# Kernel optimization log

Hardware: AMD Instinct MI355X
Metric: run time of the kernel (lower is better)

## Reference

```python
import jax, jax.numpy as jnp
import numpy as np

DIM = 1024
INTER = 512
E = 16            # n_routed_experts
TOPK = 4          # n_activated_experts
N_GROUPS = 4
TOPK_GROUPS = 2
ROUTE_SCALE = 1.0
INIT_STD = 0.02
B, S = 2, 1024


def setup_inputs() -> dict:
    key = jax.random.key(0)
    ks = jax.random.split(key, 8)
    return {
        "x": jax.random.normal(ks[0], (B, S, DIM), jnp.float32),
        "gate_w": jax.random.normal(ks[1], (E, DIM), jnp.float32) * INIT_STD,
        "gate_bias": jnp.zeros((E,), jnp.float32),
        "w1": jax.random.normal(ks[2], (E, INTER, DIM), jnp.float32) * INIT_STD,
        "w2": jax.random.normal(ks[3], (E, DIM, INTER), jnp.float32) * INIT_STD,
        "w3": jax.random.normal(ks[4], (E, INTER, DIM), jnp.float32) * INIT_STD,
        "ws1": jax.random.normal(ks[5], (INTER, DIM), jnp.float32) * INIT_STD,
        "ws2": jax.random.normal(ks[6], (DIM, INTER), jnp.float32) * INIT_STD,
        "ws3": jax.random.normal(ks[7], (INTER, DIM), jnp.float32) * INIT_STD,
    }


def reference(x, gate_w, gate_bias, w1, w2, w3, ws1, ws2, ws3):
    Bx, Sx, D = x.shape
    T = Bx * Sx
    xf = x.reshape(T, D)

    # ---- Gate: sigmoid scores + expert bias, group-limited top-k ----
    scores = jax.nn.sigmoid(xf @ gate_w.T)          # [T, E]
    original_scores = scores
    s = scores + gate_bias                          # bias only affects selection
    sg = s.reshape(T, N_GROUPS, E // N_GROUPS)
    group_scores = sg.max(axis=-1)                  # [T, G]
    _, gidx = jax.lax.top_k(group_scores, TOPK_GROUPS)
    keep = jnp.zeros((T, N_GROUPS), bool).at[jnp.arange(T)[:, None], gidx].set(True)
    s_masked = jnp.where(keep[:, :, None], sg, -jnp.inf).reshape(T, E)
    _, idx = jax.lax.top_k(s_masked, TOPK)          # [T, topk]
    weights = jnp.take_along_axis(original_scores, idx, axis=1) * ROUTE_SCALE

    # combine weights as sparse [T, E] matrix (scatter of top-k weights)
    comb = jnp.zeros((T, E), x.dtype).at[jnp.arange(T)[:, None], idx].add(weights)

    # ---- Routed experts: SwiGLU per expert, weighted combine ----
    h1 = jnp.einsum('td,eid->tei', xf, w1)          # [T, E, inter]
    h3 = jnp.einsum('td,eid->tei', xf, w3)
    h = jax.nn.silu(h1) * h3
    y = jnp.einsum('tei,edi,te->td', h, w2, comb)   # weighted combine

    # ---- Shared expert (SwiGLU MLP) ----
    z = (jax.nn.silu(xf @ ws1.T) * (xf @ ws3.T)) @ ws2.T

    return (y + z).reshape(Bx, Sx, D)
```

## Files before the change

kernel.cpp:

```cpp
#include <hip/hip_runtime.h>

#define T_TOK  2048
#define DIMD   1024
#define INTERI 512
#define NEXP   16
#define NSEG   17

typedef __bf16 bf16x8 __attribute__((ext_vector_type(8)));
typedef float  f32x4  __attribute__((ext_vector_type(4)));

#define SW(row, c) ((((c) + ((row) >> 1)) & 3) * 8)

__device__ __forceinline__ unsigned short f2b(float f) {
    union { float f; unsigned int u; } c; c.f = f;
    unsigned int u = c.u;
    unsigned int r = (u + 0x7FFFu + ((u >> 16) & 1u)) >> 16;
    return (unsigned short)r;
}

__device__ __forceinline__ void lds_barrier() {
    asm volatile("s_waitcnt lgkmcnt(0)" ::: "memory");
    __builtin_amdgcn_s_barrier();
}

__global__ __launch_bounds__(256) void cvt_all_kernel(
    const float* __restrict__ x,  const float* __restrict__ w1,
    const float* __restrict__ w3, const float* __restrict__ w2,
    const float* __restrict__ ws1, const float* __restrict__ ws3,
    const float* __restrict__ ws2,
    unsigned short* __restrict__ xb,  unsigned short* __restrict__ w1b,
    unsigned short* __restrict__ w3b, unsigned short* __restrict__ w2b,
    unsigned short* __restrict__ ws1b, unsigned short* __restrict__ ws3b,
    unsigned short* __restrict__ ws2b)
{
    int g = blockIdx.x * 256 + threadIdx.x;
    const float* s; unsigned short* d; int i;
    if      (g < 524288)  { s = x;   d = xb;   i = g; }
    else if (g < 2621440) { s = w1;  d = w1b;  i = g - 524288; }
    else if (g < 4718592) { s = w3;  d = w3b;  i = g - 2621440; }
    else if (g < 6815744) { s = w2;  d = w2b;  i = g - 4718592; }
    else if (g < 6946816) { s = ws1; d = ws1b; i = g - 6815744; }
    else if (g < 7077888) { s = ws3; d = ws3b; i = g - 6946816; }
    else                  { s = ws2; d = ws2b; i = g - 7077888; }
    float4 v = ((const float4*)s)[i];
    ushort4 o;
    o.x = f2b(v.x); o.y = f2b(v.y); o.z = f2b(v.z); o.w = f2b(v.w);
    ((ushort4*)d)[i] = o;
}

__global__ __launch_bounds__(256) void gate_score_kernel(
    const float* __restrict__ x, const float* __restrict__ gw,
    const float* __restrict__ gb,
    unsigned* __restrict__ sel, float4* __restrict__ selw)
{
    int tok  = blockIdx.x * 4 + (threadIdx.x >> 6);
    int lane = threadIdx.x & 63;
    const float* xp = x + (size_t)tok * DIMD;
    float xv[16];
#pragma unroll
    for (int j = 0; j < 16; ++j) xv[j] = xp[j * 64 + lane];

    float sc[16];
#pragma unroll
    for (int e = 0; e < 16; ++e) {
        const float* gwe = gw + e * DIMD;
        float p0 = 0.f, p1 = 0.f;
#pragma unroll
        for (int j = 0; j < 16; j += 2) {
            p0 += xv[j]     * gwe[j * 64 + lane];
            p1 += xv[j + 1] * gwe[(j + 1) * 64 + lane];
        }
        float p = p0 + p1;
#pragma unroll
        for (int o = 32; o; o >>= 1) p += __shfl_xor(p, o, 64);
        sc[e] = p;
    }
    if (lane != 0) return;

    float orig[16], s[16];
#pragma unroll
    for (int e = 0; e < 16; ++e) {
        orig[e] = 1.f / (1.f + expf(-sc[e]));
        s[e] = orig[e] + gb[e];
    }
    float gmax[4];
#pragma unroll
    for (int g = 0; g < 4; ++g) {
        float m = s[4 * g];
        for (int j = 1; j < 4; ++j) m = fmaxf(m, s[4 * g + j]);
        gmax[g] = m;
    }
    int g0 = 0;
    for (int g = 1; g < 4; ++g) if (gmax[g] > gmax[g0]) g0 = g;
    int g1 = -1;
    for (int g = 0; g < 4; ++g) { if (g == g0) continue; if (g1 < 0 || gmax[g] > gmax[g1]) g1 = g; }
    unsigned keep = (0xFu << (4 * g0)) | (0xFu << (4 * g1));
    unsigned used = 0;
    unsigned pk = 0;
    float w4[4];
    for (int j = 0; j < 4; ++j) {
        int best = -1;
        for (int e = 0; e < 16; ++e) {
            if (!((keep >> e) & 1u) || ((used >> e) & 1u)) continue;
            if (best < 0 || s[e] > s[best]) best = e;
        }
        used |= 1u << best;
        pk |= ((unsigned)best) << (4 * j);
        w4[j] = orig[best];
    }
    sel[tok] = pk;
    selw[tok] = make_float4(w4[0], w4[1], w4[2], w4[3]);
}

__global__ __launch_bounds__(256) void build_lists_kernel(
    const unsigned* __restrict__ sel, const float4* __restrict__ selw,
    int* __restrict__ counts, int* __restrict__ lst, float* __restrict__ lstw)
{
    const int e    = blockIdx.x;
    const int tid  = threadIdx.x;
    const int wave = tid >> 6;
    const int lane = tid & 63;

    __shared__ int wsum[4];
    __shared__ int basev;
    if (tid == 0) basev = 0;
    __syncthreads();

    for (int c = 0; c < T_TOK / 256; ++c) {
        int t = c * 256 + tid;
        unsigned s = sel[t];
        int match = -1;
#pragma unroll
        for (int j = 0; j < 4; ++j)
            if (((s >> (4 * j)) & 15u) == (unsigned)e) match = j;
        unsigned long long m = __ballot(match >= 0);
        int wpre = __popcll(m & ((1ull << lane) - 1ull));
        if (lane == 0) wsum[wave] = __popcll(m);
        __syncthreads();
        int pre = basev;
        for (int wv = 0; wv < wave; ++wv) pre += wsum[wv];
        if (match >= 0) {
            int pos = pre + wpre;
            lst [e * T_TOK + pos] = t | (match << 16);
            const float* wp = (const float*)&selw[t];
            lstw[e * T_TOK + pos] = wp[match];
        }
        __syncthreads();
        if (tid == 0) basev += wsum[0] + wsum[1] + wsum[2] + wsum[3];
        __syncthreads();
    }
    if (tid == 0) counts[e] = basev;
}

__global__ __launch_bounds__(256, 2) void gemm1_kernel(
    const unsigned short* __restrict__ xb,
    const unsigned short* __restrict__ w1b,
    const unsigned short* __restrict__ w3b,
    const unsigned short* __restrict__ ws1b,
    const unsigned short* __restrict__ ws3b,
    const int* __restrict__ counts,
    const int* __restrict__ lst,
    unsigned short* __restrict__ H)
{
    int b = blockIdx.x;
    int seg, mt, nt;
    if (b < 1024) {
        int xcd = b & 7, slot = b >> 3;
        seg = xcd + 8 * (slot >> 6);
        int tile = slot & 63;
        mt = tile >> 2; nt = tile & 3;
    } else {
        seg = NEXP;
        int tile = b - 1024;
        mt = tile >> 2; nt = tile & 3;
    }
    const int n_e = (seg == NEXP) ? T_TOK : counts[seg];
    const int m0  = mt * 128;
    if (m0 >= n_e) return;
    const int n0  = nt * 128;

    const unsigned short* w1p = (seg == NEXP) ? ws1b : w1b + (size_t)seg * INTERI * DIMD;
    const unsigned short* w3p = (seg == NEXP) ? ws3b : w3b + (size_t)seg * INTERI * DIMD;
    const int* lste = lst + seg * T_TOK;

    __shared__ __align__(16) unsigned short lA [2][128][32];
    __shared__ __align__(16) unsigned short lB1[2][128][32];
    __shared__ __align__(16) unsigned short lB3[2][128][32];

    const int tid  = threadIdx.x;
    const int wave = tid >> 6;
    const int lane = tid & 63;
    const int quad = lane >> 4;
    const int lrow = lane & 15;
    const int r4   = tid >> 2;
    const int ct   = tid & 3;

    int ra0 = m0 + r4;       if (ra0 > n_e - 1) ra0 = n_e - 1;
    int ra1 = m0 + r4 + 64;  if (ra1 > n_e - 1) ra1 = n_e - 1;
    int tok0 = (seg == NEXP) ? ra0 : (lste[ra0] & 0xFFFF);
    int tok1 = (seg == NEXP) ? ra1 : (lste[ra1] & 0xFFFF);
    const unsigned short* gA0  = xb  + (size_t)tok0 * DIMD + ct * 8;
    const unsigned short* gA1  = xb  + (size_t)tok1 * DIMD + ct * 8;
    const unsigned short* gB1a = w1p + (size_t)(n0 + r4)      * DIMD + ct * 8;
    const unsigned short* gB1b = w1p + (size_t)(n0 + r4 + 64) * DIMD + ct * 8;
    const unsigned short* gB3a = w3p + (size_t)(n0 + r4)      * DIMD + ct * 8;
    const unsigned short* gB3b = w3p + (size_t)(n0 + r4 + 64) * DIMD + ct * 8;

    bf16x8 pa[2][2], pb1[2][2], pb3[2][2];

#define G1LOAD(k0) do { _Pragma("unroll") for (int kk = 0; kk < 2; ++kk) { \
    pa [0][kk] = *(const bf16x8*)(gA0  + (k0) + kk * 32); \
    pa [1][kk] = *(const bf16x8*)(gA1  + (k0) + kk * 32); \
    pb1[0][kk] = *(const bf16x8*)(gB1a + (k0) + kk * 32); \
    pb1[1][kk] = *(const bf16x8*)(gB1b + (k0) + kk * 32); \
    pb3[0][kk] = *(const bf16x8*)(gB3a + (k0) + kk * 32); \
    pb3[1][kk] = *(const bf16x8*)(gB3b + (k0) + kk * 32); } } while (0)

#define G1STORE() do { _Pragma("unroll") for (int kk = 0; kk < 2; ++kk) { \
    *(bf16x8*)&lA [kk][r4]     [SW(r4, ct)]      = pa [0][kk]; \
    *(bf16x8*)&lA [kk][64 + r4][SW(64 + r4, ct)] = pa [1][kk]; \
    *(bf16x8*)&lB1[kk][r4]     [SW(r4, ct)]      = pb1[0][kk]; \
    *(bf16x8*)&lB1[kk][64 + r4][SW(64 + r4, ct)] = pb1[1][kk]; \
    *(bf16x8*)&lB3[kk][r4]     [SW(r4, ct)]      = pb3[0][kk]; \
    *(bf16x8*)&lB3[kk][64 + r4][SW(64 + r4, ct)] = pb3[1][kk]; } } while (0)

    f32x4 acc1[4][4], acc3[4][4];
    const f32x4 zero = {0.f, 0.f, 0.f, 0.f};
#pragma unroll
    for (int i = 0; i < 4; ++i)
#pragma unroll
        for (int j = 0; j < 4; ++j) { acc1[i][j] = zero; acc3[i][j] = zero; }

    const int wm = (wave & 1) * 64;
    const int wn = (wave >> 1) * 64;

    G1LOAD(0);
    const int NK = DIMD / 64;
    for (int it = 0; it < NK; ++it) {
        G1STORE();
        lds_barrier();
        if (it + 1 < NK) G1LOAD((it + 1) * 64);
#pragma unroll
        for (int kk = 0; kk < 2; ++kk) {
            bf16x8 a[4], b1[4], b3[4];
#pragma unroll
            for (int t = 0; t < 4; ++t) {
                int rr = wm + t * 16 + lrow;
                a[t] = *(const bf16x8*)&lA[kk][rr][SW(rr, quad)];
            }
#pragma unroll
            for (int t = 0; t < 4; ++t) {
                int rc = wn + t * 16 + lrow;
                b1[t] = *(const bf16x8*)&lB1[kk][rc][SW(rc, quad)];
                b3[t] = *(const bf16x8*)&lB3[kk][rc][SW(rc, quad)];
            }
#pragma unroll
            for (int i = 0; i < 4; ++i)
#pragma unroll
                for (int j = 0; j < 4; ++j) {
                    acc1[i][j] = __builtin_amdgcn_mfma_f32_16x16x32_bf16(a[i], b1[j], acc1[i][j], 0, 0, 0);
                    acc3[i][j] = __builtin_amdgcn_mfma_f32_16x16x32_bf16(a[i], b3[j], acc3[i][j], 0, 0, 0);
                }
        }
        lds_barrier();
    }
#undef G1LOAD
#undef G1STORE

    unsigned short* Hseg = H + (size_t)seg * T_TOK * INTERI;
#pragma unroll
    for (int i = 0; i < 4; ++i) {
        int rbase = m0 + wm + i * 16 + quad * 4;
#pragma unroll
        for (int r = 0; r < 4; ++r) {
            int row = rbase + r;
            if (row >= n_e) continue;
            unsigned short* hrow = Hseg + (size_t)row * INTERI + n0 + wn + lrow;
#pragma unroll
            for (int j = 0; j < 4; ++j) {
                float v1 = acc1[i][j][r];
                float v3 = acc3[i][j][r];
                float hv = (v1 / (1.f + __expf(-v1))) * v3;
                hrow[j * 16] = f2b(hv);
            }
        }
    }
}

__global__ __launch_bounds__(256, 2) void gemm2_kernel(
    const unsigned short* __restrict__ H,
    const unsigned short* __restrict__ w2b,
    const unsigned short* __restrict__ ws2b,
    const int* __restrict__ counts,
    const int* __restrict__ lst,
    const float* __restrict__ lstw,
    float* __restrict__ P)
{
    int b = blockIdx.x;
    int seg, mt, nt;
    if (b < 2048) {
        int xcd = b & 7, slot = b >> 3;
        seg = xcd + 8 * (slot >> 7);
        int tile = slot & 127;
        mt = tile >> 3; nt = tile & 7;
    } else {
        seg = NEXP;
        int tile = b - 2048;
        mt = tile >> 3; nt = tile & 7;
    }
    const int n_e = (seg == NEXP) ? T_TOK : counts[seg];
    const int m0  = mt * 128;
    if (m0 >= n_e) return;
    const int n0  = nt * 128;

    const unsigned short* w2p  = (seg == NEXP) ? ws2b : w2b + (size_t)seg * DIMD * INTERI;
    const unsigned short* Hseg = H + (size_t)seg * T_TOK * INTERI;

    __shared__ __align__(16) unsigned short lA[2][128][32];
    __shared__ __align__(16) unsigned short lB[2][128][32];

    const int tid  = threadIdx.x;
    const int wave = tid >> 6;
    const int lane = tid & 63;
    const int quad = lane >> 4;
    const int lrow = lane & 15;
    const int r4   = tid >> 2;
    const int ct   = tid & 3;

    int ra0 = m0 + r4;       if (ra0 > n_e - 1) ra0 = n_e - 1;
    int ra1 = m0 + r4 + 64;  if (ra1 > n_e - 1) ra1 = n_e - 1;
    const unsigned short* gA0 = Hseg + (size_t)ra0 * INTERI + ct * 8;
    const unsigned short* gA1 = Hseg + (size_t)ra1 * INTERI + ct * 8;
    const unsigned short* gB0 = w2p + (size_t)(n0 + r4)      * INTERI + ct * 8;
    const unsigned short* gB1 = w2p + (size_t)(n0 + r4 + 64) * INTERI + ct * 8;

    bf16x8 pa[2][2], pb[2][2];

#define G2LOAD(k0) do { _Pragma("unroll") for (int kk = 0; kk < 2; ++kk) { \
    pa[0][kk] = *(const bf16x8*)(gA0 + (k0) + kk * 32); \
    pa[1][kk] = *(const bf16x8*)(gA1 + (k0) + kk * 32); \
    pb[0][kk] = *(const bf16x8*)(gB0 + (k0) + kk * 32); \
    pb[1][kk] = *(const bf16x8*)(gB1 + (k0) + kk * 32); } } while (0)

#define G2STORE() do { _Pragma("unroll") for (int kk = 0; kk < 2; ++kk) { \
    *(bf16x8*)&lA[kk][r4]     [SW(r4, ct)]      = pa[0][kk]; \
    *(bf16x8*)&lA[kk][64 + r4][SW(64 + r4, ct)] = pa[1][kk]; \
    *(bf16x8*)&lB[kk][r4]     [SW(r4, ct)]      = pb[0][kk]; \
    *(bf16x8*)&lB[kk][64 + r4][SW(64 + r4, ct)] = pb[1][kk]; } } while (0)

    f32x4 acc[4][4];
    const f32x4 zero = {0.f, 0.f, 0.f, 0.f};
#pragma unroll
    for (int i = 0; i < 4; ++i)
#pragma unroll
        for (int j = 0; j < 4; ++j) acc[i][j] = zero;

    const int wm = (wave & 1) * 64;
    const int wn = (wave >> 1) * 64;

    G2LOAD(0);
    const int NK = INTERI / 64;
    for (int it = 0; it < NK; ++it) {
        G2STORE();
        lds_barrier();
        if (it + 1 < NK) G2LOAD((it + 1) * 64);
#pragma unroll
        for (int kk = 0; kk < 2; ++kk) {
            bf16x8 a[4], bv[4];
#pragma unroll
            for (int t = 0; t < 4; ++t) {
                int rr = wm + t * 16 + lrow;
                a[t] = *(const bf16x8*)&lA[kk][rr][SW(rr, quad)];
            }
#pragma unroll
            for (int t = 0; t < 4; ++t) {
                int rc = wn + t * 16 + lrow;
                bv[t] = *(const bf16x8*)&lB[kk][rc][SW(rc, quad)];
            }
#pragma unroll
            for (int i = 0; i < 4; ++i)
#pragma unroll
                for (int j = 0; j < 4; ++j)
                    acc[i][j] = __builtin_amdgcn_mfma_f32_16x16x32_bf16(a[i], bv[j], acc[i][j], 0, 0, 0);
        }
        lds_barrier();
    }
#undef G2LOAD
#undef G2STORE

#pragma unroll
    for (int i = 0; i < 4; ++i) {
        int rbase = m0 + wm + i * 16 + quad * 4;
#pragma unroll
        for (int r = 0; r < 4; ++r) {
            int row = rbase + r;
            if (row >= n_e) continue;
            int tok, slot; float wt;
            if (seg == NEXP) { tok = row; slot = 4; wt = 1.f; }
            else {
                int ent = lst[seg * T_TOK + row];
                tok = ent & 0xFFFF; slot = ent >> 16;
                wt = lstw[seg * T_TOK + row];
            }
            float* prow = P + ((size_t)slot * T_TOK + tok) * DIMD + n0 + wn + lrow;
#pragma unroll
            for (int j = 0; j < 4; ++j)
                prow[j * 16] = wt * acc[i][j][r];
        }
    }
}

__global__ __launch_bounds__(256) void combine_kernel(
    const float4* __restrict__ P, float4* __restrict__ y)
{
    const int i = blockIdx.x * 256 + threadIdx.x;
    const size_t plane = (size_t)T_TOK * DIMD / 4;
    float4 a = P[i];
    float4 b = P[plane + i];
    float4 c = P[2 * plane + i];
    float4 d = P[3 * plane + i];
    float4 e = P[4 * plane + i];
    float4 o;
    o.x = a.x + b.x + c.x + d.x + e.x;
    o.y = a.y + b.y + c.y + d.y + e.y;
    o.z = a.z + b.z + c.z + d.z + e.z;
    o.w = a.w + b.w + c.w + d.w + e.w;
    y[i] = o;
}

extern "C" void kernel_launch(void* const* d_in, const int* in_sizes, int n_in,
                              void* d_out, int out_size, void* d_ws, size_t ws_size,
                              hipStream_t stream)
{
    const float* x   = (const float*)d_in[0];
    const float* gw  = (const float*)d_in[1];
    const float* gb  = (const float*)d_in[2];
    const float* w1  = (const float*)d_in[3];
    const float* w2  = (const float*)d_in[4];
    const float* w3  = (const float*)d_in[5];
    const float* ws1 = (const float*)d_in[6];
    const float* ws2 = (const float*)d_in[7];
    const float* ws3 = (const float*)d_in[8];

    char* base = (char*)d_ws;
    size_t off = 0;
    auto alloc = [&](size_t bytes) {
        char* q = base + off; off += (bytes + 255) & ~(size_t)255; return q;
    };
    unsigned short* xb   = (unsigned short*)alloc((size_t)T_TOK * DIMD * 2);
    unsigned short* w1b  = (unsigned short*)alloc((size_t)NEXP * INTERI * DIMD * 2);
    unsigned short* w3b  = (unsigned short*)alloc((size_t)NEXP * INTERI * DIMD * 2);
    unsigned short* w2b  = (unsigned short*)alloc((size_t)NEXP * DIMD * INTERI * 2);
    unsigned short* ws1b = (unsigned short*)alloc((size_t)INTERI * DIMD * 2);
    unsigned short* ws3b = (unsigned short*)alloc((size_t)INTERI * DIMD * 2);
    unsigned short* ws2b = (unsigned short*)alloc((size_t)DIMD * INTERI * 2);
    unsigned short* Hb   = (unsigned short*)alloc((size_t)NSEG * T_TOK * INTERI * 2);
    int*            cnts = (int*)alloc(NEXP * 4);
    int*            lstp = (int*)alloc((size_t)NEXP * T_TOK * 4);
    float*          lstw = (float*)alloc((size_t)NEXP * T_TOK * 4);
    unsigned*       selp = (unsigned*)alloc((size_t)T_TOK * 4);
    float4*         selw = (float4*)alloc((size_t)T_TOK * 16);
    float*          Pb   = (float*)alloc((size_t)5 * T_TOK * DIMD * 4);

    cvt_all_kernel<<<28160, 256, 0, stream>>>(x, w1, w3, w2, ws1, ws3, ws2,
                                              xb, w1b, w3b, w2b, ws1b, ws3b, ws2b);
    gate_score_kernel<<<T_TOK / 4, 256, 0, stream>>>(x, gw, gb, selp, selw);
    build_lists_kernel<<<NEXP, 256, 0, stream>>>(selp, selw, cnts, lstp, lstw);
    gemm1_kernel<<<1088, 256, 0, stream>>>(xb, w1b, w3b, ws1b, ws3b, cnts, lstp, Hb);
    gemm2_kernel<<<2176, 256, 0, stream>>>(Hb, w2b, ws2b, cnts, lstp, lstw, Pb);
    combine_kernel<<<(T_TOK * DIMD / 4) / 256, 256, 0, stream>>>((const float4*)Pb, (float4*)d_out);
}
```

Measured before the change: 244.7 us.

## Fuse x conversion into gate kernel and convert w2 on the fly in gemm2

Drops the separate bf16 conversion of x and w2/ws2 from the prepass. x is now converted inside the gate kernel, which already loads it. gemm2 reads fp32 w2 directly and converts to bf16 while staging into LDS. The remaining weight conversion now writes 8 elements per thread. This cuts a full read and write pass over w2 plus one over x. In exchange gemm2 reads twice as many weight bytes per tile, and each of the several M-tiles sharing a weight tile repeats the conversion.

```diff
diff --git a/kernel.cpp b/kernel.cpp
--- a/kernel.cpp
+++ b/kernel.cpp
@@ -8,6 +8,8 @@
 
 typedef __bf16 bf16x8 __attribute__((ext_vector_type(8)));
 typedef float  f32x4  __attribute__((ext_vector_type(4)));
+typedef float  f32x8  __attribute__((ext_vector_type(8)));
+typedef unsigned short u16x8 __attribute__((ext_vector_type(8)));
 
 #define SW(row, c) ((((c) + ((row) >> 1)) & 3) * 8)
 
@@ -18,40 +20,43 @@
     return (unsigned short)r;
 }
 
+__device__ __forceinline__ bf16x8 cvt8(f32x8 v) {
+    bf16x8 r;
+#pragma unroll
+    for (int i = 0; i < 8; ++i) r[i] = (__bf16)v[i];
+    return r;
+}
+
 __device__ __forceinline__ void lds_barrier() {
     asm volatile("s_waitcnt lgkmcnt(0)" ::: "memory");
     __builtin_amdgcn_s_barrier();
 }
 
-__global__ __launch_bounds__(256) void cvt_all_kernel(
-    const float* __restrict__ x,  const float* __restrict__ w1,
-    const float* __restrict__ w3, const float* __restrict__ w2,
+__global__ __launch_bounds__(256) void cvt_w_kernel(
+    const float* __restrict__ w1,  const float* __restrict__ w3,
     const float* __restrict__ ws1, const float* __restrict__ ws3,
-    const float* __restrict__ ws2,
-    unsigned short* __restrict__ xb,  unsigned short* __restrict__ w1b,
-    unsigned short* __restrict__ w3b, unsigned short* __restrict__ w2b,
-    unsigned short* __restrict__ ws1b, unsigned short* __restrict__ ws3b,
-    unsigned short* __restrict__ ws2b)
+    unsigned short* __restrict__ w1b,  unsigned short* __restrict__ w3b,
+    unsigned short* __restrict__ ws1b, unsigned short* __restrict__ ws3b)
 {
     int g = blockIdx.x * 256 + threadIdx.x;
     const float* s; unsigned short* d; int i;
-    if      (g < 524288)  { s = x;   d = xb;   i = g; }
-    else if (g < 2621440) { s = w1;  d = w1b;  i = g - 524288; }
-    else if (g < 4718592) { s = w3;  d = w3b;  i = g - 2621440; }
-    else if (g < 6815744) { s = w2;  d = w2b;  i = g - 4718592; }
-    else if (g < 6946816) { s = ws1; d = ws1b; i = g - 6815744; }
-    else if (g < 7077888) { s = ws3; d = ws3b; i = g - 6946816; }
-    else                  { s = ws2; d = ws2b; i = g - 7077888; }
-    float4 v = ((const float4*)s)[i];
-    ushort4 o;
-    o.x = f2b(v.x); o.y = f2b(v.y); o.z = f2b(v.z); o.w = f2b(v.w);
-    ((ushort4*)d)[i] = o;
+    if      (g < 1048576) { s = w1;  d = w1b;  i = g; }
+    else if (g < 2097152) { s = w3;  d = w3b;  i = g - 1048576; }
+    else if (g < 2162688) { s = ws1; d = ws1b; i = g - 2097152; }
+    else                  { s = ws3; d = ws3b; i = g - 2162688; }
+    float4 v0 = ((const float4*)s)[2 * i];
+    float4 v1 = ((const float4*)s)[2 * i + 1];
+    u16x8 o;
+    o[0] = f2b(v0.x); o[1] = f2b(v0.y); o[2] = f2b(v0.z); o[3] = f2b(v0.w);
+    o[4] = f2b(v1.x); o[5] = f2b(v1.y); o[6] = f2b(v1.z); o[7] = f2b(v1.w);
+    ((u16x8*)d)[i] = o;
 }
 
 __global__ __launch_bounds__(256) void gate_score_kernel(
     const float* __restrict__ x, const float* __restrict__ gw,
     const float* __restrict__ gb,
-    unsigned* __restrict__ sel, float4* __restrict__ selw)
+    unsigned* __restrict__ sel, float4* __restrict__ selw,
+    unsigned short* __restrict__ xb)
 {
     int tok  = blockIdx.x * 4 + (threadIdx.x >> 6);
     int lane = threadIdx.x & 63;
@@ -59,6 +64,10 @@
     float xv[16];
 #pragma unroll
     for (int j = 0; j < 16; ++j) xv[j] = xp[j * 64 + lane];
+
+    unsigned short* xbp = xb + (size_t)tok * DIMD;
+#pragma unroll
+    for (int j = 0; j < 16; ++j) xbp[j * 64 + lane] = f2b(xv[j]);
 
     float sc[16];
 #pragma unroll
@@ -289,8 +298,8 @@
 
 __global__ __launch_bounds__(256, 2) void gemm2_kernel(
     const unsigned short* __restrict__ H,
-    const unsigned short* __restrict__ w2b,
-    const unsigned short* __restrict__ ws2b,
+    const float* __restrict__ w2f,
+    const float* __restrict__ ws2f,
     const int* __restrict__ counts,
     const int* __restrict__ lst,
     const float* __restrict__ lstw,
@@ -313,7 +322,7 @@
     if (m0 >= n_e) return;
     const int n0  = nt * 128;
 
-    const unsigned short* w2p  = (seg == NEXP) ? ws2b : w2b + (size_t)seg * DIMD * INTERI;
+    const float* w2p = (seg == NEXP) ? ws2f : w2f + (size_t)seg * DIMD * INTERI;
     const unsigned short* Hseg = H + (size_t)seg * T_TOK * INTERI;
 
     __shared__ __align__(16) unsigned short lA[2][128][32];
@@ -331,22 +340,23 @@
     int ra1 = m0 + r4 + 64;  if (ra1 > n_e - 1) ra1 = n_e - 1;
     const unsigned short* gA0 = Hseg + (size_t)ra0 * INTERI + ct * 8;
     const unsigned short* gA1 = Hseg + (size_t)ra1 * INTERI + ct * 8;
-    const unsigned short* gB0 = w2p + (size_t)(n0 + r4)      * INTERI + ct * 8;
-    const unsigned short* gB1 = w2p + (size_t)(n0 + r4 + 64) * INTERI + ct * 8;
-
-    bf16x8 pa[2][2], pb[2][2];
+    const float* gB0 = w2p + (size_t)(n0 + r4)      * INTERI + ct * 8;
+    const float* gB1 = w2p + (size_t)(n0 + r4 + 64) * INTERI + ct * 8;
+
+    bf16x8 pa[2][2];
+    f32x8  pb[2][2];
 
 #define G2LOAD(k0) do { _Pragma("unroll") for (int kk = 0; kk < 2; ++kk) { \
     pa[0][kk] = *(const bf16x8*)(gA0 + (k0) + kk * 32); \
     pa[1][kk] = *(const bf16x8*)(gA1 + (k0) + kk * 32); \
-    pb[0][kk] = *(const bf16x8*)(gB0 + (k0) + kk * 32); \
-    pb[1][kk] = *(const bf16x8*)(gB1 + (k0) + kk * 32); } } while (0)
+    pb[0][kk] = *(const f32x8*)(gB0 + (k0) + kk * 32); \
+    pb[1][kk] = *(const f32x8*)(gB1 + (k0) + kk * 32); } } while (0)
 
 #define G2STORE() do { _Pragma("unroll") for (int kk = 0; kk < 2; ++kk) { \
     *(bf16x8*)&lA[kk][r4]     [SW(r4, ct)]      = pa[0][kk]; \
     *(bf16x8*)&lA[kk][64 + r4][SW(64 + r4, ct)] = pa[1][kk]; \
-    *(bf16x8*)&lB[kk][r4]     [SW(r4, ct)]      = pb[0][kk]; \
-    *(bf16x8*)&lB[kk][64 + r4][SW(64 + r4, ct)] = pb[1][kk]; } } while (0)
+    *(bf16x8*)&lB[kk][r4]     [SW(r4, ct)]      = cvt8(pb[0][kk]); \
+    *(bf16x8*)&lB[kk][64 + r4][SW(64 + r4, ct)] = cvt8(pb[1][kk]); } } while (0)
 
     f32x4 acc[4][4];
     const f32x4 zero = {0.f, 0.f, 0.f, 0.f};
@@ -450,10 +460,8 @@
     unsigned short* xb   = (unsigned short*)alloc((size_t)T_TOK * DIMD * 2);
     unsigned short* w1b  = (unsigned short*)alloc((size_t)NEXP * INTERI * DIMD * 2);
     unsigned short* w3b  = (unsigned short*)alloc((size_t)NEXP * INTERI * DIMD * 2);
-    unsigned short* w2b  = (unsigned short*)alloc((size_t)NEXP * DIMD * INTERI * 2);
     unsigned short* ws1b = (unsigned short*)alloc((size_t)INTERI * DIMD * 2);
     unsigned short* ws3b = (unsigned short*)alloc((size_t)INTERI * DIMD * 2);
-    unsigned short* ws2b = (unsigned short*)alloc((size_t)DIMD * INTERI * 2);
     unsigned short* Hb   = (unsigned short*)alloc((size_t)NSEG * T_TOK * INTERI * 2);
     int*            cnts = (int*)alloc(NEXP * 4);
     int*            lstp = (int*)alloc((size_t)NEXP * T_TOK * 4);
@@ -462,11 +470,10 @@
     float4*         selw = (float4*)alloc((size_t)T_TOK * 16);
     float*          Pb   = (float*)alloc((size_t)5 * T_TOK * DIMD * 4);
 
-    cvt_all_kernel<<<28160, 256, 0, stream>>>(x, w1, w3, w2, ws1, ws3, ws2,
-                                              xb, w1b, w3b, w2b, ws1b, ws3b, ws2b);
-    gate_score_kernel<<<T_TOK / 4, 256, 0, stream>>>(x, gw, gb, selp, selw);
+    cvt_w_kernel<<<8704, 256, 0, stream>>>(w1, w3, ws1, ws3, w1b, w3b, ws1b, ws3b);
+    gate_score_kernel<<<T_TOK / 4, 256, 0, stream>>>(x, gw, gb, selp, selw, xb);
     build_lists_kernel<<<NEXP, 256, 0, stream>>>(selp, selw, cnts, lstp, lstw);
     gemm1_kernel<<<1088, 256, 0, stream>>>(xb, w1b, w3b, ws1b, ws3b, cnts, lstp, Hb);
-    gemm2_kernel<<<2176, 256, 0, stream>>>(Hb, w2b, ws2b, cnts, lstp, lstw, Pb);
+    gemm2_kernel<<<2176, 256, 0, stream>>>(Hb, w2, ws2, cnts, lstp, lstw, Pb);
     combine_kernel<<<(T_TOK * DIMD / 4) / 256, 256, 0, stream>>>((const float4*)Pb, (float4*)d_out);
 }
```

After: 247.5 us. Within noise of the previous version (+1.1%).

## Use direct global-to-LDS loads in GEMMs and fuse conversion with gating

Applied to the files above, without the earlier changes.

Both expert GEMM kernels now copy tiles straight from global memory into LDS with global_load_lds (16-byte) instead of staging through registers. The per-lane source column is pre-rotated so the existing LDS swizzle still holds. The register prefetch of the next tile is gone, so loads are no longer overlapped with MFMA work across iterations, and the wait and barrier now sit between each load and its compute. The weight conversion is fused with the gate-score kernel, which also converts x to bf16, and it processes 16 floats per thread to cut launches and widen stores.

```diff
diff --git a/kernel.cpp b/kernel.cpp
--- a/kernel.cpp
+++ b/kernel.cpp
@@ -8,6 +8,7 @@
 
 typedef __bf16 bf16x8 __attribute__((ext_vector_type(8)));
 typedef float  f32x4  __attribute__((ext_vector_type(4)));
+typedef unsigned short u16x8 __attribute__((ext_vector_type(8)));
 
 #define SW(row, c) ((((c) + ((row) >> 1)) & 3) * 8)
 
@@ -18,47 +19,65 @@
     return (unsigned short)r;
 }
 
-__device__ __forceinline__ void lds_barrier() {
-    asm volatile("s_waitcnt lgkmcnt(0)" ::: "memory");
-    __builtin_amdgcn_s_barrier();
-}
-
-__global__ __launch_bounds__(256) void cvt_all_kernel(
-    const float* __restrict__ x,  const float* __restrict__ w1,
-    const float* __restrict__ w3, const float* __restrict__ w2,
+__device__ __forceinline__ void glds16(const void* g, void* l) {
+    __builtin_amdgcn_global_load_lds(
+        (const __attribute__((address_space(1))) unsigned int*)g,
+        (__attribute__((address_space(3))) unsigned int*)l,
+        16, 0, 0);
+}
+
+__device__ __forceinline__ void dma_barrier() {
+    asm volatile("s_waitcnt vmcnt(0)" ::: "memory");
+    __syncthreads();
+}
+
+__global__ __launch_bounds__(256) void prep_kernel(
+    const float* __restrict__ w1,  const float* __restrict__ w3,
+    const float* __restrict__ w2,
     const float* __restrict__ ws1, const float* __restrict__ ws3,
     const float* __restrict__ ws2,
-    unsigned short* __restrict__ xb,  unsigned short* __restrict__ w1b,
-    unsigned short* __restrict__ w3b, unsigned short* __restrict__ w2b,
+    unsigned short* __restrict__ w1b,  unsigned short* __restrict__ w3b,
+    unsigned short* __restrict__ w2b,
     unsigned short* __restrict__ ws1b, unsigned short* __restrict__ ws3b,
-    unsigned short* __restrict__ ws2b)
-{
-    int g = blockIdx.x * 256 + threadIdx.x;
-    const float* s; unsigned short* d; int i;
-    if      (g < 524288)  { s = x;   d = xb;   i = g; }
-    else if (g < 2621440) { s = w1;  d = w1b;  i = g - 524288; }
-    else if (g < 4718592) { s = w3;  d = w3b;  i = g - 2621440; }
-    else if (g < 6815744) { s = w2;  d = w2b;  i = g - 4718592; }
-    else if (g < 6946816) { s = ws1; d = ws1b; i = g - 6815744; }
-    else if (g < 7077888) { s = ws3; d = ws3b; i = g - 6946816; }
-    else                  { s = ws2; d = ws2b; i = g - 7077888; }
-    float4 v = ((const float4*)s)[i];
-    ushort4 o;
-    o.x = f2b(v.x); o.y = f2b(v.y); o.z = f2b(v.z); o.w = f2b(v.w);
-    ((ushort4*)d)[i] = o;
-}
-
-__global__ __launch_bounds__(256) void gate_score_kernel(
+    unsigned short* __restrict__ ws2b,
     const float* __restrict__ x, const float* __restrict__ gw,
     const float* __restrict__ gb,
-    unsigned* __restrict__ sel, float4* __restrict__ selw)
-{
-    int tok  = blockIdx.x * 4 + (threadIdx.x >> 6);
+    unsigned* __restrict__ sel, float4* __restrict__ selw,
+    unsigned short* __restrict__ xb)
+{
+    const int b = blockIdx.x;
+    if (b < 6528) {
+        int g = b * 256 + threadIdx.x;
+        const float* s; unsigned short* d; int i;
+        if      (g < 524288)  { s = w1;  d = w1b;  i = g; }
+        else if (g < 1048576) { s = w3;  d = w3b;  i = g - 524288; }
+        else if (g < 1572864) { s = w2;  d = w2b;  i = g - 1048576; }
+        else if (g < 1605632) { s = ws1; d = ws1b; i = g - 1572864; }
+        else if (g < 1638400) { s = ws3; d = ws3b; i = g - 1605632; }
+        else                  { s = ws2; d = ws2b; i = g - 1638400; }
+        float4 v0 = ((const float4*)s)[4 * i];
+        float4 v1 = ((const float4*)s)[4 * i + 1];
+        float4 v2 = ((const float4*)s)[4 * i + 2];
+        float4 v3 = ((const float4*)s)[4 * i + 3];
+        u16x8 o0, o1;
+        o0[0] = f2b(v0.x); o0[1] = f2b(v0.y); o0[2] = f2b(v0.z); o0[3] = f2b(v0.w);
+        o0[4] = f2b(v1.x); o0[5] = f2b(v1.y); o0[6] = f2b(v1.z); o0[7] = f2b(v1.w);
+        o1[0] = f2b(v2.x); o1[1] = f2b(v2.y); o1[2] = f2b(v2.z); o1[3] = f2b(v2.w);
+        o1[4] = f2b(v3.x); o1[5] = f2b(v3.y); o1[6] = f2b(v3.z); o1[7] = f2b(v3.w);
+        ((u16x8*)d)[2 * i]     = o0;
+        ((u16x8*)d)[2 * i + 1] = o1;
+        return;
+    }
+    int tok  = (b - 6528) * 4 + (threadIdx.x >> 6);
     int lane = threadIdx.x & 63;
     const float* xp = x + (size_t)tok * DIMD;
     float xv[16];
 #pragma unroll
     for (int j = 0; j < 16; ++j) xv[j] = xp[j * 64 + lane];
+
+    unsigned short* xbp = xb + (size_t)tok * DIMD;
+#pragma unroll
+    for (int j = 0; j < 16; ++j) xbp[j * 64 + lane] = f2b(xv[j]);
 
     float sc[16];
 #pragma unroll
@@ -192,37 +211,37 @@
     const int lane = tid & 63;
     const int quad = lane >> 4;
     const int lrow = lane & 15;
-    const int r4   = tid >> 2;
-    const int ct   = tid & 3;
-
-    int ra0 = m0 + r4;       if (ra0 > n_e - 1) ra0 = n_e - 1;
-    int ra1 = m0 + r4 + 64;  if (ra1 > n_e - 1) ra1 = n_e - 1;
-    int tok0 = (seg == NEXP) ? ra0 : (lste[ra0] & 0xFFFF);
-    int tok1 = (seg == NEXP) ? ra1 : (lste[ra1] & 0xFFFF);
-    const unsigned short* gA0  = xb  + (size_t)tok0 * DIMD + ct * 8;
-    const unsigned short* gA1  = xb  + (size_t)tok1 * DIMD + ct * 8;
-    const unsigned short* gB1a = w1p + (size_t)(n0 + r4)      * DIMD + ct * 8;
-    const unsigned short* gB1b = w1p + (size_t)(n0 + r4 + 64) * DIMD + ct * 8;
-    const unsigned short* gB3a = w3p + (size_t)(n0 + r4)      * DIMD + ct * 8;
-    const unsigned short* gB3b = w3p + (size_t)(n0 + r4 + 64) * DIMD + ct * 8;
-
-    bf16x8 pa[2][2], pb1[2][2], pb3[2][2];
-
-#define G1LOAD(k0) do { _Pragma("unroll") for (int kk = 0; kk < 2; ++kk) { \
-    pa [0][kk] = *(const bf16x8*)(gA0  + (k0) + kk * 32); \
-    pa [1][kk] = *(const bf16x8*)(gA1  + (k0) + kk * 32); \
-    pb1[0][kk] = *(const bf16x8*)(gB1a + (k0) + kk * 32); \
-    pb1[1][kk] = *(const bf16x8*)(gB1b + (k0) + kk * 32); \
-    pb3[0][kk] = *(const bf16x8*)(gB3a + (k0) + kk * 32); \
-    pb3[1][kk] = *(const bf16x8*)(gB3b + (k0) + kk * 32); } } while (0)
-
-#define G1STORE() do { _Pragma("unroll") for (int kk = 0; kk < 2; ++kk) { \
-    *(bf16x8*)&lA [kk][r4]     [SW(r4, ct)]      = pa [0][kk]; \
-    *(bf16x8*)&lA [kk][64 + r4][SW(64 + r4, ct)] = pa [1][kk]; \
-    *(bf16x8*)&lB1[kk][r4]     [SW(r4, ct)]      = pb1[0][kk]; \
-    *(bf16x8*)&lB1[kk][64 + r4][SW(64 + r4, ct)] = pb1[1][kk]; \
-    *(bf16x8*)&lB3[kk][r4]     [SW(r4, ct)]      = pb3[0][kk]; \
-    *(bf16x8*)&lB3[kk][64 + r4][SW(64 + r4, ct)] = pb3[1][kk]; } } while (0)
+
+    const int lr  = lane >> 2;
+    const int lsl = lane & 3;
+    const int r0  = wave * 32 + lr, r1 = r0 + 16;
+    const int c0  = (lsl - (r0 >> 1)) & 3;
+    const int c1  = (lsl - (r1 >> 1)) & 3;
+    int ga0 = m0 + r0; if (ga0 > n_e - 1) ga0 = n_e - 1;
+    int ga1 = m0 + r1; if (ga1 > n_e - 1) ga1 = n_e - 1;
+    const int tA0 = (seg == NEXP) ? ga0 : (lste[ga0] & 0xFFFF);
+    const int tA1 = (seg == NEXP) ? ga1 : (lste[ga1] & 0xFFFF);
+    const unsigned short* pA0  = xb  + (size_t)tA0 * DIMD + c0 * 8;
+    const unsigned short* pA1  = xb  + (size_t)tA1 * DIMD + c1 * 8;
+    const unsigned short* pB10 = w1p + (size_t)(n0 + r0) * DIMD + c0 * 8;
+    const unsigned short* pB11 = w1p + (size_t)(n0 + r1) * DIMD + c1 * 8;
+    const unsigned short* pB30 = w3p + (size_t)(n0 + r0) * DIMD + c0 * 8;
+    const unsigned short* pB31 = w3p + (size_t)(n0 + r1) * DIMD + c1 * 8;
+
+#define G1STAGE(k0) do { \
+    glds16(pA0  + (k0),      &lA [0][wave * 32][0]); \
+    glds16(pA0  + (k0) + 32, &lA [1][wave * 32][0]); \
+    glds16(pA1  + (k0),      &lA [0][wave * 32 + 16][0]); \
+    glds16(pA1  + (k0) + 32, &lA [1][wave * 32 + 16][0]); \
+    glds16(pB10 + (k0),      &lB1[0][wave * 32][0]); \
+    glds16(pB10 + (k0) + 32, &lB1[1][wave * 32][0]); \
+    glds16(pB11 + (k0),      &lB1[0][wave * 32 + 16][0]); \
+    glds16(pB11 + (k0) + 32, &lB1[1][wave * 32 + 16][0]); \
+    glds16(pB30 + (k0),      &lB3[0][wave * 32][0]); \
+    glds16(pB30 + (k0) + 32, &lB3[1][wave * 32][0]); \
+    glds16(pB31 + (k0),      &lB3[0][wave * 32 + 16][0]); \
+    glds16(pB31 + (k0) + 32, &lB3[1][wave * 32 + 16][0]); \
+} while (0)
 
     f32x4 acc1[4][4], acc3[4][4];
     const f32x4 zero = {0.f, 0.f, 0.f, 0.f};
@@ -234,15 +253,13 @@
     const int wm = (wave & 1) * 64;
     const int wn = (wave >> 1) * 64;
 
-    G1LOAD(0);
     const int NK = DIMD / 64;
     for (int it = 0; it < NK; ++it) {
-        G1STORE();
-        lds_barrier();
-        if (it + 1 < NK) G1LOAD((it + 1) * 64);
+        G1STAGE(it * 64);
+        dma_barrier();
 #pragma unroll
         for (int kk = 0; kk < 2; ++kk) {
-            bf16x8 a[4], b1[4], b3[4];
+            bf16x8 a[4], bv[4];
 #pragma unroll
             for (int t = 0; t < 4; ++t) {
                 int rr = wm + t * 16 + lrow;
@@ -251,21 +268,27 @@
 #pragma unroll
             for (int t = 0; t < 4; ++t) {
                 int rc = wn + t * 16 + lrow;
-                b1[t] = *(const bf16x8*)&lB1[kk][rc][SW(rc, quad)];
-                b3[t] = *(const bf16x8*)&lB3[kk][rc][SW(rc, quad)];
+                bv[t] = *(const bf16x8*)&lB1[kk][rc][SW(rc, quad)];
             }
 #pragma unroll
             for (int i = 0; i < 4; ++i)
 #pragma unroll
-                for (int j = 0; j < 4; ++j) {
-                    acc1[i][j] = __builtin_amdgcn_mfma_f32_16x16x32_bf16(a[i], b1[j], acc1[i][j], 0, 0, 0);
-                    acc3[i][j] = __builtin_amdgcn_mfma_f32_16x16x32_bf16(a[i], b3[j], acc3[i][j], 0, 0, 0);
-                }
-        }
-        lds_barrier();
-    }
-#undef G1LOAD
-#undef G1STORE
+                for (int j = 0; j < 4; ++j)
+                    acc1[i][j] = __builtin_amdgcn_mfma_f32_16x16x32_bf16(a[i], bv[j], acc1[i][j], 0, 0, 0);
+#pragma unroll
+            for (int t = 0; t < 4; ++t) {
+                int rc = wn + t * 16 + lrow;
+                bv[t] = *(const bf16x8*)&lB3[kk][rc][SW(rc, quad)];
+            }
+#pragma unroll
+            for (int i = 0; i < 4; ++i)
+#pragma unroll
+                for (int j = 0; j < 4; ++j)
+                    acc3[i][j] = __builtin_amdgcn_mfma_f32_16x16x32_bf16(a[i], bv[j], acc3[i][j], 0, 0, 0);
+        }
+        __syncthreads();
+    }
+#undef G1STAGE
 
     unsigned short* Hseg = H + (size_t)seg * T_TOK * INTERI;
 #pragma unroll
@@ -324,29 +347,29 @@
     const int lane = tid & 63;
     const int quad = lane >> 4;
     const int lrow = lane & 15;
-    const int r4   = tid >> 2;
-    const int ct   = tid & 3;
-
-    int ra0 = m0 + r4;       if (ra0 > n_e - 1) ra0 = n_e - 1;
-    int ra1 = m0 + r4 + 64;  if (ra1 > n_e - 1) ra1 = n_e - 1;
-    const unsigned short* gA0 = Hseg + (size_t)ra0 * INTERI + ct * 8;
-    const unsigned short* gA1 = Hseg + (size_t)ra1 * INTERI + ct * 8;
-    const unsigned short* gB0 = w2p + (size_t)(n0 + r4)      * INTERI + ct * 8;
-    const unsigned short* gB1 = w2p + (size_t)(n0 + r4 + 64) * INTERI + ct * 8;
-
-    bf16x8 pa[2][2], pb[2][2];
-
-#define G2LOAD(k0) do { _Pragma("unroll") for (int kk = 0; kk < 2; ++kk) { \
-    pa[0][kk] = *(const bf16x8*)(gA0 + (k0) + kk * 32); \
-    pa[1][kk] = *(const bf16x8*)(gA1 + (k0) + kk * 32); \
-    pb[0][kk] = *(const bf16x8*)(gB0 + (k0) + kk * 32); \
-    pb[1][kk] = *(const bf16x8*)(gB1 + (k0) + kk * 32); } } while (0)
-
-#define G2STORE() do { _Pragma("unroll") for (int kk = 0; kk < 2; ++kk) { \
-    *(bf16x8*)&lA[kk][r4]     [SW(r4, ct)]      = pa[0][kk]; \
-    *(bf16x8*)&lA[kk][64 + r4][SW(64 + r4, ct)] = pa[1][kk]; \
-    *(bf16x8*)&lB[kk][r4]     [SW(r4, ct)]      = pb[0][kk]; \
-    *(bf16x8*)&lB[kk][64 + r4][SW(64 + r4, ct)] = pb[1][kk]; } } while (0)
+
+    const int lr  = lane >> 2;
+    const int lsl = lane & 3;
+    const int r0  = wave * 32 + lr, r1 = r0 + 16;
+    const int c0  = (lsl - (r0 >> 1)) & 3;
+    const int c1  = (lsl - (r1 >> 1)) & 3;
+    int ga0 = m0 + r0; if (ga0 > n_e - 1) ga0 = n_e - 1;
+    int ga1 = m0 + r1; if (ga1 > n_e - 1) ga1 = n_e - 1;
+    const unsigned short* pA0 = Hseg + (size_t)ga0 * INTERI + c0 * 8;
+    const unsigned short* pA1 = Hseg + (size_t)ga1 * INTERI + c1 * 8;
+    const unsigned short* pB0 = w2p + (size_t)(n0 + r0) * INTERI + c0 * 8;
+    const unsigned short* pB1 = w2p + (size_t)(n0 + r1) * INTERI + c1 * 8;
+
+#define G2STAGE(k0) do { \
+    glds16(pA0 + (k0),      &lA[0][wave * 32][0]); \
+    glds16(pA0 + (k0) + 32, &lA[1][wave * 32][0]); \
+    glds16(pA1 + (k0),      &lA[0][wave * 32 + 16][0]); \
+    glds16(pA1 + (k0) + 32, &lA[1][wave * 32 + 16][0]); \
+    glds16(pB0 + (k0),      &lB[0][wave * 32][0]); \
+    glds16(pB0 + (k0) + 32, &lB[1][wave * 32][0]); \
+    glds16(pB1 + (k0),      &lB[0][wave * 32 + 16][0]); \
+    glds16(pB1 + (k0) + 32, &lB[1][wave * 32 + 16][0]); \
+} while (0)
 
     f32x4 acc[4][4];
     const f32x4 zero = {0.f, 0.f, 0.f, 0.f};
@@ -358,12 +381,10 @@
     const int wm = (wave & 1) * 64;
     const int wn = (wave >> 1) * 64;
 
-    G2LOAD(0);
     const int NK = INTERI / 64;
     for (int it = 0; it < NK; ++it) {
-        G2STORE();
-        lds_barrier();
-        if (it + 1 < NK) G2LOAD((it + 1) * 64);
+        G2STAGE(it * 64);
+        dma_barrier();
 #pragma unroll
         for (int kk = 0; kk < 2; ++kk) {
             bf16x8 a[4], bv[4];
@@ -383,10 +404,9 @@
                 for (int j = 0; j < 4; ++j)
                     acc[i][j] = __builtin_amdgcn_mfma_f32_16x16x32_bf16(a[i], bv[j], acc[i][j], 0, 0, 0);
         }
-        lds_barrier();
-    }
-#undef G2LOAD
-#undef G2STORE
+        __syncthreads();
+    }
+#undef G2STAGE
 
 #pragma unroll
     for (int i = 0; i < 4; ++i) {
@@ -462,9 +482,9 @@
     float4*         selw = (float4*)alloc((size_t)T_TOK * 16);
     float*          Pb   = (float*)alloc((size_t)5 * T_TOK * DIMD * 4);
 
-    cvt_all_kernel<<<28160, 256, 0, stream>>>(x, w1, w3, w2, ws1, ws3, ws2,
-                                              xb, w1b, w3b, w2b, ws1b, ws3b, ws2b);
-    gate_score_kernel<<<T_TOK / 4, 256, 0, stream>>>(x, gw, gb, selp, selw);
+    prep_kernel<<<7040, 256, 0, stream>>>(w1, w3, w2, ws1, ws3, ws2,
+                                          w1b, w3b, w2b, ws1b, ws3b, ws2b,
+                                          x, gw, gb, selp, selw, xb);
     build_lists_kernel<<<NEXP, 256, 0, stream>>>(selp, selw, cnts, lstp, lstw);
     gemm1_kernel<<<1088, 256, 0, stream>>>(xb, w1b, w3b, ws1b, ws3b, cnts, lstp, Hb);
     gemm2_kernel<<<2176, 256, 0, stream>>>(Hb, w2b, ws2b, cnts, lstp, lstw, Pb);
```

Result: no change. 242.3 us (-1.0%).
